# Kernel tuning notes

Hardware: AMD Instinct MI355X
Metric: run time of the kernel (lower is better)

## Reference

```python
import jax, jax.numpy as jnp
import numpy as np

NEG = 1e12  # matches the torch '-inf' surrogate value


def _sinusoidal_pos(seq_len, dim):
    # bert4keras-style: pe[..., 0::2] = sin, pe[..., 1::2] = cos
    pos = jnp.arange(seq_len, dtype=jnp.float32)
    i = jnp.arange(dim // 2, dtype=jnp.float32)
    freq = jnp.power(10000.0, -2.0 * i / dim)
    ang = pos[:, None] * freq[None, :]                      # [S, dim/2]
    pe = jnp.stack([jnp.sin(ang), jnp.cos(ang)], axis=-1)   # [S, dim/2, 2]
    return pe.reshape(seq_len, dim)                          # [S, dim]


def _rope(e, cos_pos, sin_pos):
    # additional_part = stack([-e[...,1::2], e[...,::2]], -1).reshape(e.shape)
    rot = jnp.stack([-e[..., 1::2], e[..., 0::2]], axis=-1).reshape(e.shape)
    return e * cos_pos + rot * sin_pos


def setup_inputs() -> dict:
    key = jax.random.key(0)
    k = jax.random.split(key, 5)
    B, S, H, inner, L = 8, 512, 768, 64, 16
    x = jax.random.normal(k[0], (B, S, H), dtype=jnp.float32)
    W1 = jax.random.normal(k[1], (H, 2 * inner), dtype=jnp.float32) * 0.02
    b1 = jnp.zeros((2 * inner,), dtype=jnp.float32)
    W2 = jax.random.normal(k[2], (H, 2 * L), dtype=jnp.float32) * 0.02
    b2 = jnp.zeros((2 * L,), dtype=jnp.float32)
    attention_mask = jnp.ones((B, S), dtype=jnp.int32)
    return {"x": x, "W1": W1, "b1": b1, "W2": W2, "b2": b2,
            "attention_mask": attention_mask}


def reference(x, W1, b1, W2, b2, attention_mask):
    B, S, H = x.shape
    inner = W1.shape[1] // 2

    t = x @ W1 + b1                                 # [B,S,2*inner]
    start_token = t[..., 0::2]                      # [B,S,inner]
    end_token = t[..., 1::2]                        # [B,S,inner]

    pe = _sinusoidal_pos(S, inner)[None]            # [1,S,inner]
    cos_pos = jnp.repeat(pe[..., 1::2], 2, axis=-1)
    sin_pos = jnp.repeat(pe[..., 0::2], 2, axis=-1)
    start_token = _rope(start_token, cos_pos, sin_pos)
    end_token = _rope(end_token, cos_pos, sin_pos)

    span_score = jnp.einsum('bmd,bnd->bmn', start_token, end_token) / (inner ** 0.5)

    typing = jnp.swapaxes(x @ W2 + b2, 1, 2) / 2.0  # [B,2L,S]

    # entity_score: [B, L, S(start), S(end)]
    entity_score = (span_score[:, None]
                    + typing[:, 0::2, None, :]
                    + typing[:, 1::2, :, None])

    m = attention_mask.astype(entity_score.dtype)
    m_row = m[:, None, :, None]                     # mask over start axis
    m_col = m[:, None, None, :]                     # mask over end axis
    entity_score = entity_score * m_row + (-NEG) * (1.0 - m_row)
    entity_score = entity_score * m_col + (-NEG) * (1.0 - m_col)

    tril = jnp.tril(jnp.ones((S, S), entity_score.dtype), k=-1)
    entity_score = entity_score - tril * NEG
    return entity_score
```

## Files before the change

kernel.cpp:

```cpp
#include <hip/hip_runtime.h>

#define NEGF 1.0e12f

constexpr int Hdim = 768;
constexpr int NC   = 160;
constexpr int ROWS = 4096;
constexpr int SEQ  = 512;

__global__ __launch_bounds__(256) void gemm_partial_k(
    const float* __restrict__ x, const float* __restrict__ W1,
    const float* __restrict__ W2, float* __restrict__ partial)
{
    __shared__ float xs[32][33];
    __shared__ float ws[32][NC];

    const int tid = threadIdx.x;
    const int r0  = blockIdx.x * 32;
    const int kc  = blockIdx.y;
    const int k0  = kc * 384;
    const int cg  = tid & 31;
    const int rg  = tid >> 5;

    float acc[4][5];
#pragma unroll
    for (int i = 0; i < 4; i++)
#pragma unroll
        for (int j = 0; j < 5; j++) acc[i][j] = 0.0f;

    for (int kt = 0; kt < 384; kt += 32) {
        const int kbase = k0 + kt;
        {
            const int row = tid >> 3;
            const int k4  = (tid & 7) << 2;
            float4 v = *(const float4*)(x + (size_t)(r0 + row) * Hdim + kbase + k4);
            xs[row][k4 + 0] = v.x; xs[row][k4 + 1] = v.y;
            xs[row][k4 + 2] = v.z; xs[row][k4 + 3] = v.w;
        }
#pragma unroll
        for (int rep = 0; rep < 20; rep++) {
            int idx = rep * 256 + tid;
            int k   = idx / NC;
            int c   = idx - k * NC;
            float w = (c < 128) ? W1[(size_t)(kbase + k) * 128 + c]
                                : W2[(size_t)(kbase + k) * 32 + (c - 128)];
            ws[k][c] = w;
        }
        __syncthreads();

        for (int kk = 0; kk < 32; kk++) {
            float xv[4], wv[5];
#pragma unroll
            for (int i = 0; i < 4; i++) xv[i] = xs[rg * 4 + i][kk];
#pragma unroll
            for (int j = 0; j < 5; j++) wv[j] = ws[kk][cg * 5 + j];
#pragma unroll
            for (int i = 0; i < 4; i++)
#pragma unroll
                for (int j = 0; j < 5; j++) acc[i][j] += xv[i] * wv[j];
        }
        __syncthreads();
    }

    float* dst = partial + (size_t)kc * ROWS * NC;
#pragma unroll
    for (int i = 0; i < 4; i++) {
        size_t roff = (size_t)(r0 + rg * 4 + i) * NC + cg * 5;
#pragma unroll
        for (int j = 0; j < 5; j++) dst[roff + j] = acc[i][j];
    }
}

__global__ __launch_bounds__(256) void combine_rope_k(
    const float* __restrict__ partial, const float* __restrict__ b1,
    const float* __restrict__ b2, float* __restrict__ startW,
    float* __restrict__ endW, float* __restrict__ tyn,
    float* __restrict__ tym)
{
    const int tid = threadIdx.x;
    const int row = blockIdx.x * 4 + (tid >> 6);
    const int u   = tid & 63;
    const int b   = row >> 9;
    const int s   = row & 511;
    const float* p0 = partial + (size_t)row * NC;
    const float* p1 = partial + (size_t)ROWS * NC + (size_t)row * NC;

    if (u < 32) {
        const int i = u;
        float4 a0 = *(const float4*)(p0 + 4 * i);
        float4 a1 = *(const float4*)(p1 + 4 * i);
        float t0 = a0.x + a1.x + b1[4 * i + 0];
        float t1 = a0.y + a1.y + b1[4 * i + 1];
        float t2 = a0.z + a1.z + b1[4 * i + 2];
        float t3 = a0.w + a1.w + b1[4 * i + 3];
        float freq = powf(10000.0f, -(float)i * (1.0f / 32.0f));
        float ang  = (float)s * freq;
        float sn = sinf(ang), cs = cosf(ang);
        float so0 = t0 * cs - t2 * sn;
        float so1 = t2 * cs + t0 * sn;
        float eo0 = t1 * cs - t3 * sn;
        float eo1 = t3 * cs + t1 * sn;
        *(float2*)(startW + (size_t)row * 64 + 2 * i) = make_float2(so0, so1);
        *(float2*)(endW   + (size_t)row * 64 + 2 * i) = make_float2(eo0, eo1);
    } else {
        const int j = u - 32;
        float t = p0[128 + j] + p1[128 + j] + b2[j];
        float v = t * 0.5f;
        const int l = j >> 1;
        if ((j & 1) == 0) tyn[((size_t)b * 16 + l) * SEQ + s] = v;
        else              tym[((size_t)b * 16 + l) * SEQ + s] = v;
    }
}

__global__ __launch_bounds__(256) void entity_k(
    const float* __restrict__ startW, const float* __restrict__ endW,
    const float* __restrict__ tyn, const float* __restrict__ tym,
    const int* __restrict__ amask, float* __restrict__ out)
{
    __shared__ float sA[64][65];
    __shared__ float sB[64][65];
    __shared__ float tyn_s[16][64];
    __shared__ float tym_s[16][64];
    __shared__ float sp[64 * 64];
    __shared__ float mrow[64];
    __shared__ float mcol[64];

    const int tid = threadIdx.x;
    const int b   = blockIdx.z;
    const int m0  = blockIdx.y * 64;
    const int n0  = blockIdx.x * 64;

    for (int t = tid; t < 64 * 16; t += 256) {
        int m  = t >> 4;
        int k4 = (t & 15) << 2;
        float4 v = *(const float4*)(startW + (size_t)(b * SEQ + m0 + m) * 64 + k4);
        sA[m][k4] = v.x; sA[m][k4 + 1] = v.y; sA[m][k4 + 2] = v.z; sA[m][k4 + 3] = v.w;
        float4 w = *(const float4*)(endW + (size_t)(b * SEQ + n0 + m) * 64 + k4);
        sB[m][k4] = w.x; sB[m][k4 + 1] = w.y; sB[m][k4 + 2] = w.z; sB[m][k4 + 3] = w.w;
    }
    for (int t = tid; t < 16 * 64; t += 256) {
        int l = t >> 6, i = t & 63;
        tym_s[l][i] = tym[((size_t)b * 16 + l) * SEQ + m0 + i];
        tyn_s[l][i] = tyn[((size_t)b * 16 + l) * SEQ + n0 + i];
    }
    if (tid < 64)       mrow[tid] = (float)amask[b * SEQ + m0 + tid];
    else if (tid < 128) mcol[tid - 64] = (float)amask[b * SEQ + n0 + (tid - 64)];
    __syncthreads();

    {
        const int ng = tid & 15, mg = tid >> 4;
        float acc[4][4];
#pragma unroll
        for (int i = 0; i < 4; i++)
#pragma unroll
            for (int j = 0; j < 4; j++) acc[i][j] = 0.0f;

        for (int k = 0; k < 64; k++) {
            float a[4], bv[4];
#pragma unroll
            for (int i = 0; i < 4; i++) a[i] = sA[mg * 4 + i][k];
#pragma unroll
            for (int j = 0; j < 4; j++) bv[j] = sB[ng * 4 + j][k];
#pragma unroll
            for (int i = 0; i < 4; i++)
#pragma unroll
                for (int j = 0; j < 4; j++) acc[i][j] += a[i] * bv[j];
        }
#pragma unroll
        for (int i = 0; i < 4; i++)
#pragma unroll
            for (int j = 0; j < 4; j++)
                sp[(mg * 4 + i) * 64 + ng * 4 + j] = acc[i][j] * 0.125f;
    }
    __syncthreads();

    {
        const int nq = tid & 15, mo = tid >> 4;
        float mc[4], cadd[4];
#pragma unroll
        for (int q = 0; q < 4; q++) {
            mc[q]   = mcol[nq * 4 + q];
            cadd[q] = -NEGF * (1.0f - mc[q]);
        }
        for (int l = 0; l < 16; l++) {
            float4 tn = *(const float4*)&tyn_s[l][nq * 4];
            const size_t obase = (size_t)(b * 16 + l) * SEQ;
#pragma unroll
            for (int pass = 0; pass < 4; pass++) {
                int m  = pass * 16 + mo;
                int gm = m0 + m;
                float tm   = tym_s[l][m];
                float mr   = mrow[m];
                float radd = -NEGF * (1.0f - mr);
                float4 spv = *(const float4*)&sp[m * 64 + nq * 4];
                float v0 = spv.x + tn.x + tm;
                float v1 = spv.y + tn.y + tm;
                float v2 = spv.z + tn.z + tm;
                float v3 = spv.w + tn.w + tm;
                v0 = v0 * mr + radd; v1 = v1 * mr + radd;
                v2 = v2 * mr + radd; v3 = v3 * mr + radd;
                v0 = v0 * mc[0] + cadd[0]; v1 = v1 * mc[1] + cadd[1];
                v2 = v2 * mc[2] + cadd[2]; v3 = v3 * mc[3] + cadd[3];
                int gn = n0 + nq * 4;
                if (gm > gn)     v0 -= NEGF;
                if (gm > gn + 1) v1 -= NEGF;
                if (gm > gn + 2) v2 -= NEGF;
                if (gm > gn + 3) v3 -= NEGF;
                *(float4*)(out + (obase + gm) * SEQ + gn) = make_float4(v0, v1, v2, v3);
            }
        }
    }
}

extern "C" void kernel_launch(void* const* d_in, const int* in_sizes, int n_in,
                              void* d_out, int out_size, void* d_ws, size_t ws_size,
                              hipStream_t stream) {
    const float* x     = (const float*)d_in[0];
    const float* W1    = (const float*)d_in[1];
    const float* b1    = (const float*)d_in[2];
    const float* W2    = (const float*)d_in[3];
    const float* b2    = (const float*)d_in[4];
    const int*   amask = (const int*)d_in[5];
    float* out = (float*)d_out;

    float* ws      = (float*)d_ws;
    float* partial = ws;
    float* startW  = partial + 2 * ROWS * NC;
    float* endW    = startW + ROWS * 64;
    float* tyn     = endW + ROWS * 64;
    float* tym     = tyn + 8 * 16 * SEQ;

    hipLaunchKernelGGL(gemm_partial_k, dim3(128, 2), dim3(256), 0, stream,
                       x, W1, W2, partial);
    hipLaunchKernelGGL(combine_rope_k, dim3(ROWS / 4), dim3(256), 0, stream,
                       partial, b1, b2, startW, endW, tyn, tym);
    hipLaunchKernelGGL(entity_k, dim3(8, 8, 8), dim3(256), 0, stream,
                       startW, endW, tyn, tym, amask, out);
}
```

Measured before the change: 200.2 us.

## Use bf16 MFMA for projection and span GEMMs with 4-way K split

Replaces the scalar FP32 projection GEMM and span-score GEMM with bf16 MFMA 16x16x32 instructions. Inputs are converted to bf16 when staged into shared memory, and the rope outputs are stored as bf16 with the 1/8 scale folded into the start tokens. The projection now splits K four ways across 64-row tiles. The entity epilogue writes directly from the MFMA accumulators, and fast sincos/pow intrinsics are used. This trades precision (bf16 inputs) for matrix-core throughput. The output write bandwidth (B·L·S·S floats) likely still dominates.

```diff
diff --git a/kernel.cpp b/kernel.cpp
--- a/kernel.cpp
+++ b/kernel.cpp
@@ -6,74 +6,96 @@
 constexpr int NC   = 160;
 constexpr int ROWS = 4096;
 constexpr int SEQ  = 512;
-
-__global__ __launch_bounds__(256) void gemm_partial_k(
+constexpr int KSPLIT = 4;
+
+typedef __attribute__((ext_vector_type(8))) short  short8;
+typedef __attribute__((ext_vector_type(4))) float  floatx4;
+
+__device__ inline unsigned short f2bf(float f) {
+    union { float f; unsigned u; } v; v.f = f;
+    return (unsigned short)((v.u + 0x8000u) >> 16);
+}
+
+__global__ __launch_bounds__(256) void gemm_mfma_k(
     const float* __restrict__ x, const float* __restrict__ W1,
     const float* __restrict__ W2, float* __restrict__ partial)
 {
-    __shared__ float xs[32][33];
-    __shared__ float ws[32][NC];
-
-    const int tid = threadIdx.x;
-    const int r0  = blockIdx.x * 32;
-    const int kc  = blockIdx.y;
-    const int k0  = kc * 384;
-    const int cg  = tid & 31;
-    const int rg  = tid >> 5;
-
-    float acc[4][5];
-#pragma unroll
-    for (int i = 0; i < 4; i++)
-#pragma unroll
-        for (int j = 0; j < 5; j++) acc[i][j] = 0.0f;
-
-    for (int kt = 0; kt < 384; kt += 32) {
-        const int kbase = k0 + kt;
+    __shared__ __align__(16) unsigned short xs[64 * 40];
+    __shared__ __align__(16) unsigned short ws[NC * 40];
+
+    const int tid  = threadIdx.x;
+    const int wave = tid >> 6;
+    const int lane = tid & 63;
+    const int quad = lane >> 4;
+    const int nl   = lane & 15;
+    const int r0   = blockIdx.x * 64;
+    const int k0   = blockIdx.y * 192;
+
+    floatx4 acc[10];
+#pragma unroll
+    for (int t = 0; t < 10; t++) acc[t] = (floatx4)(0.0f);
+
+    for (int kt = 0; kt < 192; kt += 32) {
+        const int kb = k0 + kt;
         {
-            const int row = tid >> 3;
-            const int k4  = (tid & 7) << 2;
-            float4 v = *(const float4*)(x + (size_t)(r0 + row) * Hdim + kbase + k4);
-            xs[row][k4 + 0] = v.x; xs[row][k4 + 1] = v.y;
-            xs[row][k4 + 2] = v.z; xs[row][k4 + 3] = v.w;
-        }
-#pragma unroll
-        for (int rep = 0; rep < 20; rep++) {
-            int idx = rep * 256 + tid;
-            int k   = idx / NC;
-            int c   = idx - k * NC;
-            float w = (c < 128) ? W1[(size_t)(kbase + k) * 128 + c]
-                                : W2[(size_t)(kbase + k) * 32 + (c - 128)];
-            ws[k][c] = w;
+            const int row = tid >> 2;
+            const int kq  = (tid & 3) * 8;
+            const float* xp = x + (size_t)(r0 + row) * Hdim + kb + kq;
+            float4 v0 = *(const float4*)xp;
+            float4 v1 = *(const float4*)(xp + 4);
+            short8 sv;
+            sv[0] = (short)f2bf(v0.x); sv[1] = (short)f2bf(v0.y);
+            sv[2] = (short)f2bf(v0.z); sv[3] = (short)f2bf(v0.w);
+            sv[4] = (short)f2bf(v1.x); sv[5] = (short)f2bf(v1.y);
+            sv[6] = (short)f2bf(v1.z); sv[7] = (short)f2bf(v1.w);
+            *(short8*)(xs + row * 40 + kq) = sv;
+        }
+#pragma unroll
+        for (int g = 0; g < 3; g++) {
+            const int c   = g * 64 + (tid & 63);
+            const int kq2 = (tid >> 6) * 8;
+            if (c < NC) {
+                float f[8];
+                if (c < 128) {
+                    const float* wp = W1 + (size_t)(kb + kq2) * 128 + c;
+#pragma unroll
+                    for (int j = 0; j < 8; j++) f[j] = wp[j * 128];
+                } else {
+                    const float* wp = W2 + (size_t)(kb + kq2) * 32 + (c - 128);
+#pragma unroll
+                    for (int j = 0; j < 8; j++) f[j] = wp[j * 32];
+                }
+                short8 sv;
+#pragma unroll
+                for (int j = 0; j < 8; j++) sv[j] = (short)f2bf(f[j]);
+                *(short8*)(ws + c * 40 + kq2) = sv;
+            }
         }
         __syncthreads();
 
-        for (int kk = 0; kk < 32; kk++) {
-            float xv[4], wv[5];
-#pragma unroll
-            for (int i = 0; i < 4; i++) xv[i] = xs[rg * 4 + i][kk];
-#pragma unroll
-            for (int j = 0; j < 5; j++) wv[j] = ws[kk][cg * 5 + j];
-#pragma unroll
-            for (int i = 0; i < 4; i++)
-#pragma unroll
-                for (int j = 0; j < 5; j++) acc[i][j] += xv[i] * wv[j];
+        short8 af = *(const short8*)(xs + (wave * 16 + nl) * 40 + quad * 8);
+#pragma unroll
+        for (int t = 0; t < 10; t++) {
+            short8 bf = *(const short8*)(ws + (t * 16 + nl) * 40 + quad * 8);
+            acc[t] = __builtin_amdgcn_mfma_f32_16x16x32_bf16(af, bf, acc[t], 0, 0, 0);
         }
         __syncthreads();
     }
 
-    float* dst = partial + (size_t)kc * ROWS * NC;
-#pragma unroll
-    for (int i = 0; i < 4; i++) {
-        size_t roff = (size_t)(r0 + rg * 4 + i) * NC + cg * 5;
-#pragma unroll
-        for (int j = 0; j < 5; j++) dst[roff + j] = acc[i][j];
+    float* pout = partial + (size_t)blockIdx.y * ROWS * NC;
+#pragma unroll
+    for (int t = 0; t < 10; t++) {
+#pragma unroll
+        for (int r = 0; r < 4; r++) {
+            pout[(size_t)(r0 + wave * 16 + quad * 4 + r) * NC + t * 16 + nl] = acc[t][r];
+        }
     }
 }
 
 __global__ __launch_bounds__(256) void combine_rope_k(
     const float* __restrict__ partial, const float* __restrict__ b1,
-    const float* __restrict__ b2, float* __restrict__ startW,
-    float* __restrict__ endW, float* __restrict__ tyn,
+    const float* __restrict__ b2, unsigned short* __restrict__ startbf,
+    unsigned short* __restrict__ endbf, float* __restrict__ tyn,
     float* __restrict__ tym)
 {
     const int tid = threadIdx.x;
@@ -82,28 +104,34 @@
     const int b   = row >> 9;
     const int s   = row & 511;
     const float* p0 = partial + (size_t)row * NC;
-    const float* p1 = partial + (size_t)ROWS * NC + (size_t)row * NC;
+    const size_t cstride = (size_t)ROWS * NC;
 
     if (u < 32) {
         const int i = u;
         float4 a0 = *(const float4*)(p0 + 4 * i);
-        float4 a1 = *(const float4*)(p1 + 4 * i);
-        float t0 = a0.x + a1.x + b1[4 * i + 0];
-        float t1 = a0.y + a1.y + b1[4 * i + 1];
-        float t2 = a0.z + a1.z + b1[4 * i + 2];
-        float t3 = a0.w + a1.w + b1[4 * i + 3];
-        float freq = powf(10000.0f, -(float)i * (1.0f / 32.0f));
+        float4 a1 = *(const float4*)(p0 + cstride + 4 * i);
+        float4 a2 = *(const float4*)(p0 + 2 * cstride + 4 * i);
+        float4 a3 = *(const float4*)(p0 + 3 * cstride + 4 * i);
+        float t0 = a0.x + a1.x + a2.x + a3.x + b1[4 * i + 0];
+        float t1 = a0.y + a1.y + a2.y + a3.y + b1[4 * i + 1];
+        float t2 = a0.z + a1.z + a2.z + a3.z + b1[4 * i + 2];
+        float t3 = a0.w + a1.w + a2.w + a3.w + b1[4 * i + 3];
+        float freq = __powf(10000.0f, -(float)i * (1.0f / 32.0f));
         float ang  = (float)s * freq;
-        float sn = sinf(ang), cs = cosf(ang);
-        float so0 = t0 * cs - t2 * sn;
-        float so1 = t2 * cs + t0 * sn;
+        float sn, cs;
+        __sincosf(ang, &sn, &cs);
+        float so0 = (t0 * cs - t2 * sn) * 0.125f;
+        float so1 = (t2 * cs + t0 * sn) * 0.125f;
         float eo0 = t1 * cs - t3 * sn;
         float eo1 = t3 * cs + t1 * sn;
-        *(float2*)(startW + (size_t)row * 64 + 2 * i) = make_float2(so0, so1);
-        *(float2*)(endW   + (size_t)row * 64 + 2 * i) = make_float2(eo0, eo1);
+        ushort2 sp; sp.x = f2bf(so0); sp.y = f2bf(so1);
+        ushort2 ep; ep.x = f2bf(eo0); ep.y = f2bf(eo1);
+        *(ushort2*)(startbf + (size_t)row * 64 + 2 * i) = sp;
+        *(ushort2*)(endbf   + (size_t)row * 64 + 2 * i) = ep;
     } else {
         const int j = u - 32;
-        float t = p0[128 + j] + p1[128 + j] + b2[j];
+        float t = p0[128 + j] + p0[cstride + 128 + j] + p0[2 * cstride + 128 + j]
+                + p0[3 * cstride + 128 + j] + b2[j];
         float v = t * 0.5f;
         const int l = j >> 1;
         if ((j & 1) == 0) tyn[((size_t)b * 16 + l) * SEQ + s] = v;
@@ -112,100 +140,90 @@
 }
 
 __global__ __launch_bounds__(256) void entity_k(
-    const float* __restrict__ startW, const float* __restrict__ endW,
+    const unsigned short* __restrict__ startbf, const unsigned short* __restrict__ endbf,
     const float* __restrict__ tyn, const float* __restrict__ tym,
     const int* __restrict__ amask, float* __restrict__ out)
 {
-    __shared__ float sA[64][65];
-    __shared__ float sB[64][65];
-    __shared__ float tyn_s[16][64];
-    __shared__ float tym_s[16][64];
-    __shared__ float sp[64 * 64];
-    __shared__ float mrow[64];
-    __shared__ float mcol[64];
+    __shared__ __align__(16) unsigned short sA[64 * 72];
+    __shared__ __align__(16) unsigned short sB[64 * 72];
+    __shared__ float tyn_s[16 * 64];
+    __shared__ float tym_s[16 * 64];
+    __shared__ float mrow_s[64];
+    __shared__ float mcol_s[64];
 
     const int tid = threadIdx.x;
     const int b   = blockIdx.z;
     const int m0  = blockIdx.y * 64;
     const int n0  = blockIdx.x * 64;
 
-    for (int t = tid; t < 64 * 16; t += 256) {
-        int m  = t >> 4;
-        int k4 = (t & 15) << 2;
-        float4 v = *(const float4*)(startW + (size_t)(b * SEQ + m0 + m) * 64 + k4);
-        sA[m][k4] = v.x; sA[m][k4 + 1] = v.y; sA[m][k4 + 2] = v.z; sA[m][k4 + 3] = v.w;
-        float4 w = *(const float4*)(endW + (size_t)(b * SEQ + n0 + m) * 64 + k4);
-        sB[m][k4] = w.x; sB[m][k4 + 1] = w.y; sB[m][k4 + 2] = w.z; sB[m][k4 + 3] = w.w;
+    for (int t = tid; t < 512; t += 256) {
+        int row = t >> 3;
+        int kq  = (t & 7) * 8;
+        *(short8*)(sA + row * 72 + kq) =
+            *(const short8*)(startbf + (size_t)(b * SEQ + m0 + row) * 64 + kq);
+        *(short8*)(sB + row * 72 + kq) =
+            *(const short8*)(endbf + (size_t)(b * SEQ + n0 + row) * 64 + kq);
     }
     for (int t = tid; t < 16 * 64; t += 256) {
         int l = t >> 6, i = t & 63;
-        tym_s[l][i] = tym[((size_t)b * 16 + l) * SEQ + m0 + i];
-        tyn_s[l][i] = tyn[((size_t)b * 16 + l) * SEQ + n0 + i];
-    }
-    if (tid < 64)       mrow[tid] = (float)amask[b * SEQ + m0 + tid];
-    else if (tid < 128) mcol[tid - 64] = (float)amask[b * SEQ + n0 + (tid - 64)];
+        tym_s[t] = tym[((size_t)b * 16 + l) * SEQ + m0 + i];
+        tyn_s[t] = tyn[((size_t)b * 16 + l) * SEQ + n0 + i];
+    }
+    if (tid < 64)       mrow_s[tid] = (float)amask[b * SEQ + m0 + tid];
+    else if (tid < 128) mcol_s[tid - 64] = (float)amask[b * SEQ + n0 + (tid - 64)];
     __syncthreads();
 
-    {
-        const int ng = tid & 15, mg = tid >> 4;
-        float acc[4][4];
-#pragma unroll
-        for (int i = 0; i < 4; i++)
-#pragma unroll
-            for (int j = 0; j < 4; j++) acc[i][j] = 0.0f;
-
-        for (int k = 0; k < 64; k++) {
-            float a[4], bv[4];
-#pragma unroll
-            for (int i = 0; i < 4; i++) a[i] = sA[mg * 4 + i][k];
-#pragma unroll
-            for (int j = 0; j < 4; j++) bv[j] = sB[ng * 4 + j][k];
-#pragma unroll
-            for (int i = 0; i < 4; i++)
-#pragma unroll
-                for (int j = 0; j < 4; j++) acc[i][j] += a[i] * bv[j];
-        }
-#pragma unroll
-        for (int i = 0; i < 4; i++)
-#pragma unroll
-            for (int j = 0; j < 4; j++)
-                sp[(mg * 4 + i) * 64 + ng * 4 + j] = acc[i][j] * 0.125f;
-    }
-    __syncthreads();
-
-    {
-        const int nq = tid & 15, mo = tid >> 4;
-        float mc[4], cadd[4];
-#pragma unroll
-        for (int q = 0; q < 4; q++) {
-            mc[q]   = mcol[nq * 4 + q];
-            cadd[q] = -NEGF * (1.0f - mc[q]);
-        }
-        for (int l = 0; l < 16; l++) {
-            float4 tn = *(const float4*)&tyn_s[l][nq * 4];
-            const size_t obase = (size_t)(b * 16 + l) * SEQ;
-#pragma unroll
-            for (int pass = 0; pass < 4; pass++) {
-                int m  = pass * 16 + mo;
-                int gm = m0 + m;
-                float tm   = tym_s[l][m];
-                float mr   = mrow[m];
-                float radd = -NEGF * (1.0f - mr);
-                float4 spv = *(const float4*)&sp[m * 64 + nq * 4];
-                float v0 = spv.x + tn.x + tm;
-                float v1 = spv.y + tn.y + tm;
-                float v2 = spv.z + tn.z + tm;
-                float v3 = spv.w + tn.w + tm;
-                v0 = v0 * mr + radd; v1 = v1 * mr + radd;
-                v2 = v2 * mr + radd; v3 = v3 * mr + radd;
-                v0 = v0 * mc[0] + cadd[0]; v1 = v1 * mc[1] + cadd[1];
-                v2 = v2 * mc[2] + cadd[2]; v3 = v3 * mc[3] + cadd[3];
-                int gn = n0 + nq * 4;
-                if (gm > gn)     v0 -= NEGF;
-                if (gm > gn + 1) v1 -= NEGF;
-                if (gm > gn + 2) v2 -= NEGF;
-                if (gm > gn + 3) v3 -= NEGF;
-                *(float4*)(out + (obase + gm) * SEQ + gn) = make_float4(v0, v1, v2, v3);
+    const int wave = tid >> 6;
+    const int lane = tid & 63;
+    const int quad = lane >> 4;
+    const int nl   = lane & 15;
+
+    short8 a0 = *(const short8*)(sA + (wave * 16 + nl) * 72 + quad * 8);
+    short8 a1 = *(const short8*)(sA + (wave * 16 + nl) * 72 + 32 + quad * 8);
+
+    floatx4 acc[4];
+#pragma unroll
+    for (int t = 0; t < 4; t++) acc[t] = (floatx4)(0.0f);
+#pragma unroll
+    for (int t = 0; t < 4; t++) {
+        short8 bf0 = *(const short8*)(sB + (t * 16 + nl) * 72 + quad * 8);
+        short8 bf1 = *(const short8*)(sB + (t * 16 + nl) * 72 + 32 + quad * 8);
+        acc[t] = __builtin_amdgcn_mfma_f32_16x16x32_bf16(a0, bf0, acc[t], 0, 0, 0);
+        acc[t] = __builtin_amdgcn_mfma_f32_16x16x32_bf16(a1, bf1, acc[t], 0, 0, 0);
+    }
+
+    float mr[4], radd[4];
+#pragma unroll
+    for (int r = 0; r < 4; r++) {
+        mr[r]   = mrow_s[wave * 16 + quad * 4 + r];
+        radd[r] = -NEGF * (1.0f - mr[r]);
+    }
+    float mc[4], cadd[4];
+#pragma unroll
+    for (int t = 0; t < 4; t++) {
+        mc[t]   = mcol_s[t * 16 + nl];
+        cadd[t] = -NEGF * (1.0f - mc[t]);
+    }
+    const bool lower = (m0 > n0);
+    const bool diag  = (m0 == n0);
+    const int  lm    = wave * 16 + quad * 4;
+
+    for (int l = 0; l < 16; l++) {
+        float tmv[4];
+#pragma unroll
+        for (int r = 0; r < 4; r++) tmv[r] = tym_s[l * 64 + lm + r];
+        float* ob = out + ((size_t)(b * 16 + l) * SEQ + m0 + lm) * SEQ + n0;
+#pragma unroll
+        for (int t = 0; t < 4; t++) {
+            float tnv = tyn_s[l * 64 + t * 16 + nl];
+#pragma unroll
+            for (int r = 0; r < 4; r++) {
+                float v = acc[t][r] + tnv + tmv[r];
+                v = v * mr[r] + radd[r];
+                v = v * mc[t] + cadd[t];
+                if (lower) v -= NEGF;
+                else if (diag && (lm + r > t * 16 + nl)) v -= NEGF;
+                ob[(size_t)r * SEQ + t * 16 + nl] = v;
             }
         }
     }
@@ -222,17 +240,17 @@
     const int*   amask = (const int*)d_in[5];
     float* out = (float*)d_out;
 
-    float* ws      = (float*)d_ws;
-    float* partial = ws;
-    float* startW  = partial + 2 * ROWS * NC;
-    float* endW    = startW + ROWS * 64;
-    float* tyn     = endW + ROWS * 64;
-    float* tym     = tyn + 8 * 16 * SEQ;
-
-    hipLaunchKernelGGL(gemm_partial_k, dim3(128, 2), dim3(256), 0, stream,
+    char* base = (char*)d_ws;
+    float*          partial = (float*)base;
+    unsigned short* startbf = (unsigned short*)(base + 10485760);
+    unsigned short* endbf   = (unsigned short*)(base + 10485760 + 524288);
+    float*          tyn     = (float*)(base + 10485760 + 2 * 524288);
+    float*          tym     = (float*)(base + 10485760 + 2 * 524288 + 262144);
+
+    hipLaunchKernelGGL(gemm_mfma_k, dim3(64, KSPLIT), dim3(256), 0, stream,
                        x, W1, W2, partial);
     hipLaunchKernelGGL(combine_rope_k, dim3(ROWS / 4), dim3(256), 0, stream,
-                       partial, b1, b2, startW, endW, tyn, tym);
+                       partial, b1, b2, startbf, endbf, tyn, tym);
     hipLaunchKernelGGL(entity_k, dim3(8, 8, 8), dim3(256), 0, stream,
-                       startW, endW, tyn, tym, amask, out);
-}
+                       startbf, endbf, tyn, tym, amask, out);
+}
```

Measured after the change: 168.2 us. 1.19x faster.
